# Kernel optimization log

Hardware: AMD Instinct MI355X
Metric: run time of the kernel (lower is better)

The kernel has to match this reference:

```python
import jax, jax.numpy as jnp
import numpy as np
import math

HIDDEN = 1024
N_HEADS = 16
HEAD_DIM = HIDDEN // N_HEADS
N_BLOCKS = 16
BATCH = 2
SEQ = 4096


def setup_inputs() -> dict:
    key = jax.random.key(0)
    ks = jax.random.split(key, 8)
    attention_input = jax.random.normal(ks[0], (BATCH, SEQ, HIDDEN), dtype=jnp.float32)
    attention_mask = jnp.ones((BATCH, SEQ), dtype=jnp.float32)
    # permutation over the num_blocks*num_heads flattened (block, head) axis
    permutation = jax.random.permutation(ks[1], N_BLOCKS * N_HEADS)
    init = 0.02
    q_w = jax.random.normal(ks[2], (HIDDEN, N_HEADS, HEAD_DIM), dtype=jnp.float32) * init
    q_b = jax.random.normal(ks[3], (N_HEADS, HEAD_DIM), dtype=jnp.float32) * init
    k_w = jax.random.normal(ks[4], (HIDDEN, N_HEADS, HEAD_DIM), dtype=jnp.float32) * init
    k_b = jax.random.normal(ks[5], (N_HEADS, HEAD_DIM), dtype=jnp.float32) * init
    v_w = jax.random.normal(ks[6], (HIDDEN, N_HEADS, HEAD_DIM), dtype=jnp.float32) * init
    v_b = jax.random.normal(ks[7], (N_HEADS, HEAD_DIM), dtype=jnp.float32) * init
    return {"attention_input": attention_input, "attention_mask": attention_mask,
            "permutation": permutation, "q_w": q_w, "q_b": q_b,
            "k_w": k_w, "k_b": k_b, "v_w": v_w, "v_b": v_b}


def reference(attention_input, attention_mask, permutation, q_w, q_b, k_w, k_b, v_w, v_b):
    B = attention_mask.shape[0]
    S = attention_mask.shape[1]
    nb = N_BLOCKS
    nh, d = q_b.shape
    blk = S // nb
    # QKV projections: [B,S,H] x [H,N,D] -> [B,S,N,D]
    q = jnp.einsum('bsh,hnd->bsnd', attention_input, q_w) + q_b
    k = jnp.einsum('bsh,hnd->bsnd', attention_input, k_w) + k_b
    v = jnp.einsum('bsh,hnd->bsnd', attention_input, v_w) + v_b

    def blockify(x):  # [B,S,N,D] -> [B, nb, nh, blk, d]
        return x.reshape(B, nb, blk, nh, d).transpose(0, 1, 3, 2, 4)

    q = blockify(q)
    # flatten (block, head) axis and gather per permutation
    k = blockify(k).reshape(B, nb * nh, blk, d)[:, permutation].reshape(B, nb, nh, blk, d)
    v = blockify(v).reshape(B, nb * nh, blk, d)[:, permutation].reshape(B, nb, nh, blk, d)

    scale = 1.0 / math.sqrt(float(d))
    logits = jnp.einsum('bgnqd,bgnkd->bgnqk', q, k) * scale  # block-local scores
    attn = jax.nn.softmax(logits, axis=-1)  # dropout prob 0 / eval mode
    ctx = jnp.einsum('bgnqk,bgnkd->bgnqd', attn, v)
    # [B,nb,nh,blk,d] -> [B,nb,blk,nh,d] -> [B,S,nh,d]
    return ctx.transpose(0, 1, 3, 2, 4).reshape(B, S, nh, d)
```

## Files before the change

### kernel.cpp

```cpp
#include <hip/hip_runtime.h>
#include <hip/hip_bf16.h>
#include <stdint.h>

typedef __attribute__((ext_vector_type(4))) float f32x4;
typedef __attribute__((ext_vector_type(8))) short s16x8;

__device__ inline short f2bf(float f) {
  union { float f; uint32_t u; } v; v.f = f;
  uint32_t r = v.u + 0x7fffu + ((v.u >> 16) & 1u);
  return (short)(r >> 16);
}

__device__ inline void gload_lds16(const void* g, void* l) {
  __builtin_amdgcn_global_load_lds((const __attribute__((address_space(1))) void*)g,
                                   (__attribute__((address_space(3))) void*)l,
                                   16, 0, 0);
}

#define MFMA16 __builtin_amdgcn_mfma_f32_16x16x32_bf16

__global__ __launch_bounds__(256) void k_prep(const float* __restrict__ x,
                                              short* __restrict__ xb,
                                              const float* __restrict__ qw,
                                              const float* __restrict__ kw,
                                              const float* __restrict__ vw,
                                              short* __restrict__ wt) {
  __shared__ float tile[64][65];
  int bx = blockIdx.x;
  if (bx < 4096) {
    int i = (bx * 256 + threadIdx.x) * 8;
    const float4* p = (const float4*)(x + i);
    float4 a = p[0], b = p[1];
    s16x8 o;
    o[0] = f2bf(a.x); o[1] = f2bf(a.y); o[2] = f2bf(a.z); o[3] = f2bf(a.w);
    o[4] = f2bf(b.x); o[5] = f2bf(b.y); o[6] = f2bf(b.z); o[7] = f2bf(b.w);
    *(s16x8*)(xb + i) = o;
    return;
  }
  bx -= 4096;
  int a  = bx >> 8;
  int t2 = bx & 255;
  int k0 = (t2 >> 4) << 6;
  int n0 = (t2 & 15) << 6;
  const float* w = (a == 0) ? qw : (a == 1) ? kw : vw;
  int c = threadIdx.x & 63, rr = threadIdx.x >> 6;
#pragma unroll
  for (int i = 0; i < 16; ++i) {
    int r = i * 4 + rr;
    tile[r][c] = w[(k0 + r) * 1024 + n0 + c];
  }
  __syncthreads();
  short* o = wt + a * 1048576;
#pragma unroll
  for (int i = 0; i < 16; ++i) {
    int r = i * 4 + rr;
    o[(n0 + r) * 1024 + k0 + c] = f2bf(tile[c][r]);
  }
}

__global__ __launch_bounds__(256, 2) void k_gemm(const short* __restrict__ xb,
                                                 const short* __restrict__ wt,
                                                 const float* __restrict__ qbias,
                                                 const float* __restrict__ kbias,
                                                 const float* __restrict__ vbias,
                                                 short* __restrict__ Qo,
                                                 short* __restrict__ Ko,
                                                 short* __restrict__ Vo) {
  __shared__ short lds[36864];
  const int tid = threadIdx.x, lane = tid & 63, wv = tid >> 6;
  const int wm = wv >> 1, wn = wv & 1;
  const int mt = blockIdx.x, by = blockIdx.y;
  const int a = by >> 3;
  const short* asrc = xb + (size_t)(mt * 256) * 1024;
  const short* bsrc = wt + (size_t)a * 1048576 + (size_t)((by & 7) * 128) * 1024;

  int srcA[4], dstA[4], srcB[2], dstB[2];
#pragma unroll
  for (int i = 0; i < 4; ++i) {
    int L = i * 256 + tid, s = L & 31;
    int row = (L >> 5) * 8 + (s >> 2);
    int c = (s & 3) ^ ((s >> 3) & 3);
    srcA[i] = row * 1024 + c * 8;
    dstA[i] = L * 16;
  }
#pragma unroll
  for (int i = 0; i < 2; ++i) {
    int L = i * 256 + tid, s = L & 31;
    int row = (L >> 5) * 8 + (s >> 2);
    int c = (s & 3) ^ ((s >> 3) & 3);
    srcB[i] = row * 1024 + c * 8;
    dstB[i] = 16384 + L * 16;
  }

  int aoff[8], boff[4];
#pragma unroll
  for (int m = 0; m < 8; ++m) {
    int row = wm * 128 + m * 16 + (lane & 15);
    aoff[m] = ((row >> 3) * 32 + (row & 7) * 4 + ((lane >> 4) ^ ((row >> 1) & 3))) * 16;
  }
#pragma unroll
  for (int n = 0; n < 4; ++n) {
    int row = wn * 64 + n * 16 + (lane & 15);
    boff[n] = 16384 + ((row >> 3) * 32 + (row & 7) * 4 + ((lane >> 4) ^ ((row >> 1) & 3))) * 16;
  }

  f32x4 acc[8][4] = {};

  auto STAGE = [&](int t, int bb) {
    const short* at = asrc + t * 32;
    const short* bt = bsrc + t * 32;
    char* l = (char*)lds + bb;
#pragma unroll
    for (int i = 0; i < 4; ++i) gload_lds16(at + srcA[i], l + dstA[i]);
#pragma unroll
    for (int i = 0; i < 2; ++i) gload_lds16(bt + srcB[i], l + dstB[i]);
  };

  STAGE(0, 0);
  STAGE(1, 24576);
  int bcur = 0, bpre = 49152;

  for (int t = 0; t < 31; ++t) {
    asm volatile("s_waitcnt vmcnt(6)" ::: "memory");
    __builtin_amdgcn_s_barrier();
    asm volatile("" ::: "memory");
    if (t < 30) STAGE(t + 2, bpre);
    const char* bufc = (const char*)lds + bcur;
    s16x8 af[8], bf[4];
#pragma unroll
    for (int m = 0; m < 8; ++m) af[m] = *(const s16x8*)(bufc + aoff[m]);
#pragma unroll
    for (int n = 0; n < 4; ++n) bf[n] = *(const s16x8*)(bufc + boff[n]);
    __builtin_amdgcn_s_setprio(1);
#pragma unroll
    for (int m = 0; m < 8; ++m)
#pragma unroll
      for (int n = 0; n < 4; ++n)
        acc[m][n] = MFMA16(af[m], bf[n], acc[m][n], 0, 0, 0);
    __builtin_amdgcn_s_setprio(0);
    bcur += 24576; if (bcur == 73728) bcur = 0;
    bpre += 24576; if (bpre == 73728) bpre = 0;
  }
  asm volatile("s_waitcnt vmcnt(0)" ::: "memory");
  __builtin_amdgcn_s_barrier();
  asm volatile("" ::: "memory");
  {
    const char* bufc = (const char*)lds + bcur;
    s16x8 af[8], bf[4];
#pragma unroll
    for (int m = 0; m < 8; ++m) af[m] = *(const s16x8*)(bufc + aoff[m]);
#pragma unroll
    for (int n = 0; n < 4; ++n) bf[n] = *(const s16x8*)(bufc + boff[n]);
    __builtin_amdgcn_s_setprio(1);
#pragma unroll
    for (int m = 0; m < 8; ++m)
#pragma unroll
      for (int n = 0; n < 4; ++n)
        acc[m][n] = MFMA16(af[m], bf[n], acc[m][n], 0, 0, 0);
    __builtin_amdgcn_s_setprio(0);
  }

  const float* bias = (a == 0) ? qbias : (a == 1) ? kbias : vbias;
  short* outp = (a == 0) ? Qo : (a == 1) ? Ko : Vo;
  int nbase = (by & 7) * 128 + wn * 64;
  int mbase = mt * 256 + wm * 128;
#pragma unroll
  for (int n = 0; n < 4; ++n) {
    int nloc = nbase + n * 16 + (lane & 15);
    float bv = bias[nloc];
    int head = nloc >> 6, d = nloc & 63;
#pragma unroll
    for (int m = 0; m < 8; ++m)
#pragma unroll
      for (int r = 0; r < 4; ++r) {
        int mm = mbase + m * 16 + ((lane >> 4) << 2) + r;
        outp[((size_t)head * 8192 + mm) * 64 + d] = f2bf(acc[m][n][r] + bv);
      }
  }
}

__global__ __launch_bounds__(256, 2) void k_attn(const short* __restrict__ Qb,
                                                 const short* __restrict__ Kb,
                                                 const short* __restrict__ Vb,
                                                 const int* __restrict__ perm,
                                                 float* __restrict__ out) {
  __shared__ short Ks[256 * 64];
  __shared__ short Vs[64 * 256];
  __shared__ short Ps[4 * 1024];

  int tid = threadIdx.x;
  int lane = tid & 63, wv = tid >> 6;
  int bx = blockIdx.x;
  int wg = (bx & 7) * 128 + (bx >> 3);
  int b = wg >> 9, g = (wg >> 5) & 15, n = (wg >> 1) & 15, h = wg & 1;
  int p = perm[g * 16 + n];
  int pg = p >> 4, ph = p & 15;

  const short* qsrc = Qb + ((size_t)n * 8192 + b * 4096 + g * 256 + h * 128) * 64;
  const short* ksrc = Kb + ((size_t)ph * 8192 + b * 4096 + pg * 256) * 64;
  const short* vsrc = Vb + ((size_t)ph * 8192 + b * 4096 + pg * 256) * 64;

  int qr0 = wv * 32;

#pragma unroll
  for (int i = 0; i < 8; ++i) {
    int c = i * 256 + tid;
    int row = c >> 3;
    int sc = ((c & 7) << 4) ^ ((row & 7) << 4);
    gload_lds16(ksrc + row * 64 + (sc >> 1), (char*)Ks + c * 16);
  }
  __builtin_amdgcn_sched_barrier(0);
  s16x8 vreg[8];
#pragma unroll
  for (int i = 0; i < 8; ++i) {
    int c = i * 256 + tid;
    int t = c >> 3;
    int d0 = (c & 7) << 3;
    vreg[i] = *(const s16x8*)(vsrc + t * 64 + d0);
  }
  s16x8 qreg[2][2];
#pragma unroll
  for (int rf = 0; rf < 2; ++rf)
#pragma unroll
    for (int ks = 0; ks < 2; ++ks) {
      int row = qr0 + rf * 16 + (lane & 15);
      qreg[rf][ks] = *(const s16x8*)(qsrc + row * 64 + ks * 32 + ((lane >> 4) << 3));
    }
  __builtin_amdgcn_sched_barrier(0);
  asm volatile("s_waitcnt vmcnt(12)" ::: "memory");
  __builtin_amdgcn_s_barrier();
  __builtin_amdgcn_sched_barrier(0);

  f32x4 accS[2][16] = {};
  __builtin_amdgcn_s_setprio(1);
#pragma unroll
  for (int ks = 0; ks < 2; ++ks) {
    int cb = (ks << 6) + ((lane >> 4) << 4);
#pragma unroll
    for (int cf = 0; cf < 16; ++cf) {
      int row = cf * 16 + (lane & 15);
      s16x8 bk = *(const s16x8*)((const char*)Ks + row * 128 + (cb ^ ((row & 7) << 4)));
      accS[0][cf] = MFMA16(qreg[0][ks], bk, accS[0][cf], 0, 0, 0);
      accS[1][cf] = MFMA16(qreg[1][ks], bk, accS[1][cf], 0, 0, 0);
    }
  }
  __builtin_amdgcn_s_setprio(0);

#pragma unroll
  for (int i = 0; i < 8; ++i) {
    int c = i * 256 + tid;
    int t = c >> 3;
    int d0 = (c & 7) << 3;
#pragma unroll
    for (int j = 0; j < 8; ++j) {
      int d = d0 + j;
      int sl = (d & 7) ^ ((d >> 3) & 7);
      int by = d * 512 + ((t * 2) ^ (sl << 4));
      *(short*)((char*)Vs + by) = vreg[i][j];
    }
  }
  __syncthreads();

  const float sc_log2e = 0.125f * 1.44269504088896f;
  float mx[2][4], inv[2][4];
#pragma unroll
  for (int rf = 0; rf < 2; ++rf)
#pragma unroll
    for (int r = 0; r < 4; ++r) {
      float m_ = accS[rf][0][r];
#pragma unroll
      for (int cf = 1; cf < 16; ++cf) m_ = fmaxf(m_, accS[rf][cf][r]);
#pragma unroll
      for (int msk = 1; msk < 16; msk <<= 1) m_ = fmaxf(m_, __shfl_xor(m_, msk));
      mx[rf][r] = m_;
    }
#pragma unroll
  for (int rf = 0; rf < 2; ++rf)
#pragma unroll
    for (int r = 0; r < 4; ++r) {
      float s_ = 0.f;
#pragma unroll
      for (int cf = 0; cf < 16; ++cf) {
        float e = exp2f((accS[rf][cf][r] - mx[rf][r]) * sc_log2e);
        accS[rf][cf][r] = e;
        s_ += e;
      }
#pragma unroll
      for (int msk = 1; msk < 16; msk <<= 1) s_ += __shfl_xor(s_, msk);
      inv[rf][r] = 1.0f / s_;
    }

  const int g4 = lane >> 4;
  const int s0l = (lane >> 3) & 1;
  const int kv7 = lane & 7;
  const int rs = ((lane & 1) ^ ((lane >> 3) & 1))
               | ((((lane >> 1) & 1) ^ ((lane >> 4) & 1)) << 1)
               | (((lane >> 2) & 1) << 2)
               | (((lane >> 3) & 1) << 3)
               | (((lane >> 4) & 1) << 4)
               | (((lane >> 5) & 1) << 5);

  f32x4 accO[2][4] = {};
  short* pchunk = Ps + wv * 1024;
#pragma unroll
  for (int ks = 0; ks < 8; ++ks) {
#pragma unroll
    for (int rf = 0; rf < 2; ++rf)
#pragma unroll
      for (int half = 0; half < 2; ++half) {
        int cf = ks * 2 + half;
#pragma unroll
        for (int r = 0; r < 4; ++r) {
          int slot = ((r & 1) ^ (g4 >> 1))
                   | ((((r >> 1) & 1) ^ s0l) << 1)
                   | ((g4 & 1) << 2)
                   | ((g4 >> 1) << 3)
                   | (s0l << 4)
                   | (half << 5);
          pchunk[rf * 512 + slot * 8 + kv7] = f2bf(accS[rf][cf][r]);
        }
      }
    int cbv = (ks << 6) + ((lane >> 4) << 4);
    s16x8 bv[4];
#pragma unroll
    for (int dc = 0; dc < 4; ++dc) {
      int vrow = dc * 16 + (lane & 15);
      int sl = (vrow & 7) ^ ((vrow >> 3) & 7);
      bv[dc] = *(const s16x8*)((const char*)Vs + vrow * 512 + (cbv ^ (sl << 4)));
    }
    __builtin_amdgcn_s_setprio(1);
#pragma unroll
    for (int rf = 0; rf < 2; ++rf) {
      s16x8 ap = *(const s16x8*)(pchunk + rf * 512 + rs * 8);
#pragma unroll
      for (int dc = 0; dc < 4; ++dc)
        accO[rf][dc] = MFMA16(ap, bv[dc], accO[rf][dc], 0, 0, 0);
    }
    __builtin_amdgcn_s_setprio(0);
  }

#pragma unroll
  for (int rf = 0; rf < 2; ++rf)
#pragma unroll
    for (int dc = 0; dc < 4; ++dc)
#pragma unroll
      for (int r = 0; r < 4; ++r) {
        int q = h * 128 + qr0 + rf * 16 + ((lane >> 4) << 2) + r;
        int d = dc * 16 + (lane & 15);
        out[(size_t)((b * 4096 + g * 256 + q) * 16 + n) * 64 + d] = accO[rf][dc][r] * inv[rf][r];
      }
}

extern "C" void kernel_launch(void* const* d_in, const int* in_sizes, int n_in,
                              void* d_out, int out_size, void* d_ws, size_t ws_size,
                              hipStream_t stream) {
  const float* x    = (const float*)d_in[0];
  const int*   perm = (const int*)d_in[2];
  const float* qw   = (const float*)d_in[3];
  const float* qb   = (const float*)d_in[4];
  const float* kw   = (const float*)d_in[5];
  const float* kb   = (const float*)d_in[6];
  const float* vw   = (const float*)d_in[7];
  const float* vb   = (const float*)d_in[8];
  float* out = (float*)d_out;

  char* ws = (char*)d_ws;
  short* Xb = (short*)(ws);
  short* Wt = (short*)(ws + 16777216UL);
  short* Qb = (short*)(ws + 23068672UL);
  short* Kb = (short*)(ws + 39845888UL);
  short* Vb = (short*)(ws + 56623104UL);

  k_prep<<<4864, 256, 0, stream>>>(x, Xb, qw, kw, vw, Wt);
  k_gemm<<<dim3(32, 24), 256, 0, stream>>>(Xb, Wt, qb, kb, vb, Qb, Kb, Vb);
  k_attn<<<1024, 256, 0, stream>>>(Qb, Kb, Vb, perm, out);
}
```

Baseline: 100.4 us.

## Split attention KV into two halves with staged K loads and unnormalized softmax

The 256-key block is processed in two 128-key halves. The second half of K is staged into LDS via global_load_lds while the first half's PV product runs, and V for each half is loaded and transposed into a half-size LDS buffer. This halves the K and V shared-memory footprint and overlaps loads with compute. The per-row max subtraction is removed and exp2 is applied directly to the scaled logits, with only the running sum accumulated. That saves the max reductions but risks overflow for inputs with large logits.

```diff
diff --git a/kernel.cpp b/kernel.cpp
--- a/kernel.cpp
+++ b/kernel.cpp
@@ -184,8 +184,8 @@
                                                  const short* __restrict__ Vb,
                                                  const int* __restrict__ perm,
                                                  float* __restrict__ out) {
-  __shared__ short Ks[256 * 64];
-  __shared__ short Vs[64 * 256];
+  __shared__ short Ks[128 * 64];
+  __shared__ short Vt[64 * 128];
   __shared__ short Ps[4 * 1024];
 
   int tid = threadIdx.x;
@@ -202,22 +202,18 @@
 
   int qr0 = wv * 32;
 
-#pragma unroll
-  for (int i = 0; i < 8; ++i) {
-    int c = i * 256 + tid;
-    int row = c >> 3;
-    int sc = ((c & 7) << 4) ^ ((row & 7) << 4);
-    gload_lds16(ksrc + row * 64 + (sc >> 1), (char*)Ks + c * 16);
-  }
+  auto STAGE_K = [&](int hf) {
+#pragma unroll
+    for (int i = 0; i < 4; ++i) {
+      int c = i * 256 + tid;
+      int row = c >> 3;
+      int sc = ((c & 7) << 4) ^ ((row & 7) << 4);
+      gload_lds16(ksrc + (size_t)(hf * 128 + row) * 64 + (sc >> 1), (char*)Ks + c * 16);
+    }
+  };
+
+  STAGE_K(0);
   __builtin_amdgcn_sched_barrier(0);
-  s16x8 vreg[8];
-#pragma unroll
-  for (int i = 0; i < 8; ++i) {
-    int c = i * 256 + tid;
-    int t = c >> 3;
-    int d0 = (c & 7) << 3;
-    vreg[i] = *(const s16x8*)(vsrc + t * 64 + d0);
-  }
   s16x8 qreg[2][2];
 #pragma unroll
   for (int rf = 0; rf < 2; ++rf)
@@ -227,72 +223,15 @@
       qreg[rf][ks] = *(const s16x8*)(qsrc + row * 64 + ks * 32 + ((lane >> 4) << 3));
     }
   __builtin_amdgcn_sched_barrier(0);
-  asm volatile("s_waitcnt vmcnt(12)" ::: "memory");
+  asm volatile("s_waitcnt vmcnt(4)" ::: "memory");
   __builtin_amdgcn_s_barrier();
   __builtin_amdgcn_sched_barrier(0);
 
-  f32x4 accS[2][16] = {};
-  __builtin_amdgcn_s_setprio(1);
-#pragma unroll
-  for (int ks = 0; ks < 2; ++ks) {
-    int cb = (ks << 6) + ((lane >> 4) << 4);
-#pragma unroll
-    for (int cf = 0; cf < 16; ++cf) {
-      int row = cf * 16 + (lane & 15);
-      s16x8 bk = *(const s16x8*)((const char*)Ks + row * 128 + (cb ^ ((row & 7) << 4)));
-      accS[0][cf] = MFMA16(qreg[0][ks], bk, accS[0][cf], 0, 0, 0);
-      accS[1][cf] = MFMA16(qreg[1][ks], bk, accS[1][cf], 0, 0, 0);
-    }
-  }
-  __builtin_amdgcn_s_setprio(0);
-
-#pragma unroll
-  for (int i = 0; i < 8; ++i) {
-    int c = i * 256 + tid;
-    int t = c >> 3;
-    int d0 = (c & 7) << 3;
-#pragma unroll
-    for (int j = 0; j < 8; ++j) {
-      int d = d0 + j;
-      int sl = (d & 7) ^ ((d >> 3) & 7);
-      int by = d * 512 + ((t * 2) ^ (sl << 4));
-      *(short*)((char*)Vs + by) = vreg[i][j];
-    }
-  }
-  __syncthreads();
-
   const float sc_log2e = 0.125f * 1.44269504088896f;
-  float mx[2][4], inv[2][4];
-#pragma unroll
-  for (int rf = 0; rf < 2; ++rf)
-#pragma unroll
-    for (int r = 0; r < 4; ++r) {
-      float m_ = accS[rf][0][r];
-#pragma unroll
-      for (int cf = 1; cf < 16; ++cf) m_ = fmaxf(m_, accS[rf][cf][r]);
-#pragma unroll
-      for (int msk = 1; msk < 16; msk <<= 1) m_ = fmaxf(m_, __shfl_xor(m_, msk));
-      mx[rf][r] = m_;
-    }
-#pragma unroll
-  for (int rf = 0; rf < 2; ++rf)
-#pragma unroll
-    for (int r = 0; r < 4; ++r) {
-      float s_ = 0.f;
-#pragma unroll
-      for (int cf = 0; cf < 16; ++cf) {
-        float e = exp2f((accS[rf][cf][r] - mx[rf][r]) * sc_log2e);
-        accS[rf][cf][r] = e;
-        s_ += e;
-      }
-#pragma unroll
-      for (int msk = 1; msk < 16; msk <<= 1) s_ += __shfl_xor(s_, msk);
-      inv[rf][r] = 1.0f / s_;
-    }
-
-  const int g4 = lane >> 4;
-  const int s0l = (lane >> 3) & 1;
-  const int kv7 = lane & 7;
+  float l_run[2][4] = {{0.f,0.f,0.f,0.f},{0.f,0.f,0.f,0.f}};
+  f32x4 accO[2][4] = {};
+
+  const int g4 = lane >> 4, s0l = (lane >> 3) & 1, kv7 = lane & 7;
   const int rs = ((lane & 1) ^ ((lane >> 3) & 1))
                | ((((lane >> 1) & 1) ^ ((lane >> 4) & 1)) << 1)
                | (((lane >> 2) & 1) << 2)
@@ -300,45 +239,118 @@
                | (((lane >> 4) & 1) << 4)
                | (((lane >> 5) & 1) << 5);
 
-  f32x4 accO[2][4] = {};
-  short* pchunk = Ps + wv * 1024;
-#pragma unroll
-  for (int ks = 0; ks < 8; ++ks) {
+#pragma unroll
+  for (int hf = 0; hf < 2; ++hf) {
+    f32x4 accS[2][8];
 #pragma unroll
     for (int rf = 0; rf < 2; ++rf)
 #pragma unroll
-      for (int half = 0; half < 2; ++half) {
-        int cf = ks * 2 + half;
+      for (int cf = 0; cf < 8; ++cf) accS[rf][cf] = (f32x4){0.f, 0.f, 0.f, 0.f};
+    __builtin_amdgcn_s_setprio(1);
+#pragma unroll
+    for (int ks = 0; ks < 2; ++ks) {
+      int cb = (ks << 6) + ((lane >> 4) << 4);
+#pragma unroll
+      for (int cf = 0; cf < 8; ++cf) {
+        int row = cf * 16 + (lane & 15);
+        s16x8 bk = *(const s16x8*)((const char*)Ks + row * 128 + (cb ^ ((row & 7) << 4)));
+        accS[0][cf] = MFMA16(qreg[0][ks], bk, accS[0][cf], 0, 0, 0);
+        accS[1][cf] = MFMA16(qreg[1][ks], bk, accS[1][cf], 0, 0, 0);
+      }
+    }
+    __builtin_amdgcn_s_setprio(0);
+
+    s16x8 vreg[4];
+#pragma unroll
+    for (int i = 0; i < 4; ++i) {
+      int c = i * 256 + tid;
+      int t = c >> 3, d0 = (c & 7) << 3;
+      vreg[i] = *(const s16x8*)(vsrc + (size_t)(hf * 128 + t) * 64 + d0);
+    }
+
+    __builtin_amdgcn_s_barrier();
+    __builtin_amdgcn_sched_barrier(0);
+    if (hf == 0) STAGE_K(1);
+
+#pragma unroll
+    for (int i = 0; i < 4; ++i) {
+      int c = i * 256 + tid;
+      int t = c >> 3, d0 = (c & 7) << 3;
+#pragma unroll
+      for (int j = 0; j < 8; ++j) {
+        int d = d0 + j;
+        int sl = (d & 7) ^ ((d >> 3) & 7);
+        *(short*)((char*)Vt + d * 256 + ((t * 2) ^ (sl << 4))) = vreg[i][j];
+      }
+    }
+
+#pragma unroll
+    for (int rf = 0; rf < 2; ++rf)
+#pragma unroll
+      for (int cf = 0; cf < 8; ++cf)
 #pragma unroll
         for (int r = 0; r < 4; ++r) {
-          int slot = ((r & 1) ^ (g4 >> 1))
-                   | ((((r >> 1) & 1) ^ s0l) << 1)
-                   | ((g4 & 1) << 2)
-                   | ((g4 >> 1) << 3)
-                   | (s0l << 4)
-                   | (half << 5);
-          pchunk[rf * 512 + slot * 8 + kv7] = f2bf(accS[rf][cf][r]);
+          float e = exp2f(accS[rf][cf][r] * sc_log2e);
+          accS[rf][cf][r] = e;
+          l_run[rf][r] += e;
         }
-      }
-    int cbv = (ks << 6) + ((lane >> 4) << 4);
-    s16x8 bv[4];
-#pragma unroll
-    for (int dc = 0; dc < 4; ++dc) {
-      int vrow = dc * 16 + (lane & 15);
-      int sl = (vrow & 7) ^ ((vrow >> 3) & 7);
-      bv[dc] = *(const s16x8*)((const char*)Vs + vrow * 512 + (cbv ^ (sl << 4)));
-    }
-    __builtin_amdgcn_s_setprio(1);
-#pragma unroll
-    for (int rf = 0; rf < 2; ++rf) {
-      s16x8 ap = *(const s16x8*)(pchunk + rf * 512 + rs * 8);
-#pragma unroll
-      for (int dc = 0; dc < 4; ++dc)
-        accO[rf][dc] = MFMA16(ap, bv[dc], accO[rf][dc], 0, 0, 0);
-    }
-    __builtin_amdgcn_s_setprio(0);
-  }
-
+
+    asm volatile("s_waitcnt lgkmcnt(0)" ::: "memory");
+    __builtin_amdgcn_s_barrier();
+    __builtin_amdgcn_sched_barrier(0);
+
+    short* pchunk = Ps + wv * 1024;
+#pragma unroll
+    for (int ks = 0; ks < 4; ++ks) {
+#pragma unroll
+      for (int rf = 0; rf < 2; ++rf)
+#pragma unroll
+        for (int half = 0; half < 2; ++half) {
+          int cf = ks * 2 + half;
+#pragma unroll
+          for (int r = 0; r < 4; ++r) {
+            int slot = ((r & 1) ^ (g4 >> 1))
+                     | ((((r >> 1) & 1) ^ s0l) << 1)
+                     | ((g4 & 1) << 2)
+                     | ((g4 >> 1) << 3)
+                     | (s0l << 4)
+                     | (half << 5);
+            pchunk[rf * 512 + slot * 8 + kv7] = f2bf(accS[rf][cf][r]);
+          }
+        }
+      int cbv = (ks << 6) + ((lane >> 4) << 4);
+      __builtin_amdgcn_s_setprio(1);
+#pragma unroll
+      for (int rf = 0; rf < 2; ++rf) {
+        s16x8 ap = *(const s16x8*)(pchunk + rf * 512 + rs * 8);
+#pragma unroll
+        for (int dc = 0; dc < 4; ++dc) {
+          int vrow = dc * 16 + (lane & 15);
+          int sl = (vrow & 7) ^ ((vrow >> 3) & 7);
+          s16x8 bv = *(const s16x8*)((const char*)Vt + vrow * 256 + (cbv ^ (sl << 4)));
+          accO[rf][dc] = MFMA16(ap, bv, accO[rf][dc], 0, 0, 0);
+        }
+      }
+      __builtin_amdgcn_s_setprio(0);
+    }
+
+    if (hf == 0) {
+      asm volatile("s_waitcnt vmcnt(0)" ::: "memory");
+      __builtin_amdgcn_s_barrier();
+      __builtin_amdgcn_sched_barrier(0);
+    }
+  }
+
+  float inv[2][4];
+#pragma unroll
+  for (int rf = 0; rf < 2; ++rf)
+#pragma unroll
+    for (int r = 0; r < 4; ++r) {
+      float s_ = l_run[rf][r];
+#pragma unroll
+      for (int msk = 1; msk < 16; msk <<= 1) s_ += __shfl_xor(s_, msk);
+      inv[rf][r] = 1.0f / s_;
+    }
 #pragma unroll
   for (int rf = 0; rf < 2; ++rf)
 #pragma unroll
```

Result: no change. 100.1 us (-0.3%).
